# Kernel tuning notes

Hardware: AMD Instinct MI355X
Metric: run time of the kernel (lower is better)

## Reference

```python
import jax, jax.numpy as jnp
import numpy as np

NUM_HEADS = 8
KERNEL = 7  # odd, dilation = 1


def _neighbor_indices(n, k):
    # NATTEN semantics: window start clamped so the kxk window stays inside [0, n)
    r = k // 2
    starts = jnp.clip(jnp.arange(n) - r, 0, n - k)  # [n]
    return starts[:, None] + jnp.arange(k)[None, :]  # [n, k]


def setup_inputs() -> dict:
    key = jax.random.key(0)
    k1, k2, k3, k4 = jax.random.split(key, 4)
    B, H, W, C = 2, 56, 56, 256
    return {
        "x": jax.random.normal(k1, (B, H, W, C), dtype=jnp.float32),
        "w_qk": jax.random.normal(k2, (2 * C, C), dtype=jnp.float32) * 0.02,
        "w_v": jax.random.normal(k3, (C, C), dtype=jnp.float32) * 0.02,
        "w_proj": jax.random.normal(k4, (C, C), dtype=jnp.float32) * 0.02,
        "b_proj": jnp.zeros((C,), dtype=jnp.float32),
    }


def reference(x, w_qk, w_v, w_proj, b_proj):
    B, H, W, C = x.shape
    NH, K = NUM_HEADS, KERNEL
    HD = C // NH
    scale = HD ** -0.5

    # qk / v projections (torch Linear: y = x @ W.T)
    qk = (x @ w_qk.T).reshape(B, H, W, 2, NH, HD)
    q = jnp.moveaxis(qk[:, :, :, 0], 3, 1) * scale  # [B, NH, H, W, HD]
    k = jnp.moveaxis(qk[:, :, :, 1], 3, 1)          # [B, NH, H, W, HD]
    v = jnp.moveaxis((x @ w_v.T).reshape(B, H, W, NH, HD), 3, 1)  # [B, NH, H, W, HD]

    idx_h = _neighbor_indices(H, K)  # [H, K]
    idx_w = _neighbor_indices(W, K)  # [W, K]
    ih = idx_h[:, None, :, None]  # [H, 1, K, 1]
    iw = idx_w[None, :, None, :]  # [1, W, 1, K]

    # Gather per-pixel neighborhoods: [B, NH, H, W, K, K, HD]
    k_nb = k[:, :, ih, iw, :]
    v_nb = v[:, :, ih, iw, :]

    # windowed QK^T -> [B, NH, H, W, K*K]
    attn = jnp.einsum('bnijf,bnijpqf->bnijpq', q, k_nb).reshape(B, NH, H, W, K * K)
    attn = jax.nn.softmax(attn, axis=-1)

    # windowed AV -> [B, NH, H, W, HD]
    out = jnp.einsum('bnijk,bnijkf->bnijf', attn, v_nb.reshape(B, NH, H, W, K * K, HD))

    out = jnp.moveaxis(out, 1, 3).reshape(B, H, W, C)
    out = out @ w_proj.T + b_proj
    return out, attn
```

## Files before the change

### kernel.cpp

```cpp
#include <hip/hip_runtime.h>
#include <math.h>

#define Bb   2
#define Hh   56
#define Ww   56
#define Cc   256
#define NHh  8
#define HDd  32
#define KK   7
#define HWsz (Hh*Ww)
#define Mtot (Bb*Hh*Ww)

typedef __bf16 bf16x8 __attribute__((ext_vector_type(8)));
typedef float  f32x4  __attribute__((ext_vector_type(4)));

__global__ __launch_bounds__(256) void gemm_bf16(
    const float* __restrict__ A, const float* __restrict__ W0,
    const float* __restrict__ W1, float* __restrict__ Cout,
    int Kdim, int N, int n_split, int scale_below, float scale,
    const float* __restrict__ bias)
{
    __shared__ __bf16 As[4096];
    __shared__ __bf16 Bs[4096];

    const int tid = threadIdx.x;
    const int m0  = blockIdx.y * 64;
    const int n0  = blockIdx.x * 64;

    const int mm = tid >> 2;
    const int q  = tid & 3;
    const float* arow = A + (size_t)(m0 + mm) * Kdim + q * 16;
    const int n_idx = n0 + mm;
    const float* brow = (n_idx < n_split ? W0 + (size_t)n_idx * Kdim
                                         : W1 + (size_t)(n_idx - n_split) * Kdim) + q * 16;

    const int ks_st  = q >> 1;
    const int sub_st = mm >> 4;
    const int row_st = mm & 15;
    const int c0_st  = (q & 1) * 2;
    const int blk_st = ks_st * 4 + sub_st;
    const int off0 = blk_st * 512 + row_st * 32 + ((c0_st ^ (row_st & 3)) * 8);
    const int off1 = blk_st * 512 + row_st * 32 + (((c0_st + 1) ^ (row_st & 3)) * 8);

    const int w    = tid >> 6;
    const int lane = tid & 63;
    const int fr_row = lane & 15;
    const int fr_c   = lane >> 4;
    const int fr_off = fr_row * 32 + ((fr_c ^ (fr_row & 3)) * 8);

    f32x4 acc[4] = {};

    for (int k0 = 0; k0 < Kdim; k0 += 64) {
        float4 a0 = *(const float4*)(arow + k0);
        float4 a1 = *(const float4*)(arow + k0 + 4);
        float4 a2 = *(const float4*)(arow + k0 + 8);
        float4 a3 = *(const float4*)(arow + k0 + 12);
        float4 b0 = *(const float4*)(brow + k0);
        float4 b1 = *(const float4*)(brow + k0 + 4);
        float4 b2 = *(const float4*)(brow + k0 + 8);
        float4 b3 = *(const float4*)(brow + k0 + 12);
        __syncthreads();
        bf16x8 av0 = { (__bf16)a0.x, (__bf16)a0.y, (__bf16)a0.z, (__bf16)a0.w,
                       (__bf16)a1.x, (__bf16)a1.y, (__bf16)a1.z, (__bf16)a1.w };
        bf16x8 av1 = { (__bf16)a2.x, (__bf16)a2.y, (__bf16)a2.z, (__bf16)a2.w,
                       (__bf16)a3.x, (__bf16)a3.y, (__bf16)a3.z, (__bf16)a3.w };
        bf16x8 bv0 = { (__bf16)b0.x, (__bf16)b0.y, (__bf16)b0.z, (__bf16)b0.w,
                       (__bf16)b1.x, (__bf16)b1.y, (__bf16)b1.z, (__bf16)b1.w };
        bf16x8 bv1 = { (__bf16)b2.x, (__bf16)b2.y, (__bf16)b2.z, (__bf16)b2.w,
                       (__bf16)b3.x, (__bf16)b3.y, (__bf16)b3.z, (__bf16)b3.w };
        *(bf16x8*)&As[off0] = av0;
        *(bf16x8*)&As[off1] = av1;
        *(bf16x8*)&Bs[off0] = bv0;
        *(bf16x8*)&Bs[off1] = bv1;
        __syncthreads();
        #pragma unroll
        for (int ks = 0; ks < 2; ++ks) {
            bf16x8 af = *(const bf16x8*)&As[(ks * 4 + w) * 512 + fr_off];
            #pragma unroll
            for (int n = 0; n < 4; ++n) {
                bf16x8 bfr = *(const bf16x8*)&Bs[(ks * 4 + n) * 512 + fr_off];
                acc[n] = __builtin_amdgcn_mfma_f32_16x16x32_bf16(af, bfr, acc[n], 0, 0, 0);
            }
        }
    }

    #pragma unroll
    for (int n = 0; n < 4; ++n) {
        const int gcol = n0 + n * 16 + fr_row;
        const float sc_ = (gcol < scale_below) ? scale : 1.f;
        const float bs_ = bias ? bias[gcol] : 0.f;
        #pragma unroll
        for (int r = 0; r < 4; ++r) {
            const int grow = m0 + w * 16 + fr_c * 4 + r;
            Cout[(size_t)grow * N + gcol] = acc[n][r] * sc_ + bs_;
        }
    }
}

__global__ __launch_bounds__(256, 5) void nattn_84(
    const float* __restrict__ qkv, float* __restrict__ attn_out,
    float* __restrict__ attn_glob)
{
    __shared__ float Ks[140 * 36];
    __shared__ float Ss[32 * 49];

    const int bx   = blockIdx.x;
    const int head = bx & 7;
    int t = bx >> 3;
    const int tj = t % 14; t /= 14;
    const int ti = t % 7;
    const int b  = t / 7;
    const int tid = threadIdx.x;

    int base_h = ti * 8 - 3; if (base_h < 0) base_h = 0; if (base_h > Hh - 14) base_h = Hh - 14;
    int base_w = tj * 4 - 3; if (base_w < 0) base_w = 0; if (base_w > Ww - 10) base_w = Ww - 10;

    const int pixb = b * HWsz;
    const int hoff = head * 32;

    #pragma unroll
    for (int it = 0; it < 5; ++it) {
        const int idx = tid + it * 256;
        if (idx < 1120) {
            const int p = idx >> 3, c = idx & 7;
            const int pix = pixb + (base_h + p / 10) * Ww + base_w + p % 10;
            *(float4*)&Ks[p * 36 + c * 4] =
                *(const float4*)&qkv[(size_t)pix * 768 + 256 + hoff + c * 4];
        }
    }

    const int q  = tid >> 3;
    const int r  = tid & 7;
    const int qi = ti * 8 + (q >> 2);
    const int qj = tj * 4 + (q & 3);

    float4 qreg[8];
    {
        const float* qp = &qkv[(size_t)(pixb + qi * Ww + qj) * 768 + hoff];
        #pragma unroll
        for (int c = 0; c < 8; ++c) qreg[c] = *(const float4*)(qp + c * 4);
    }

    float4 vreg[5];
    #pragma unroll
    for (int it = 0; it < 5; ++it) {
        const int idx = tid + it * 256;
        if (idx < 1120) {
            const int p = idx >> 3, c = idx & 7;
            const int pix = pixb + (base_h + p / 10) * Ww + base_w + p % 10;
            vreg[it] = *(const float4*)&qkv[(size_t)pix * 768 + 512 + hoff + c * 4];
        }
    }
    __syncthreads();

    int ih0 = qi - 3; if (ih0 < 0) ih0 = 0; if (ih0 > Hh - 7) ih0 = Hh - 7;
    int iw0 = qj - 3; if (iw0 < 0) iw0 = 0; if (iw0 > Ww - 7) iw0 = Ww - 7;
    const int lh0 = ih0 - base_h, lw0 = iw0 - base_w;

    float sc[7];
    float mx = -1e30f;
    #pragma unroll
    for (int tt = 0; tt < 7; ++tt) {
        const int k = r + 8 * tt;
        if (k < 49) {
            const int krow = (lh0 + k / 7) * 10 + lw0 + k % 7;
            const float* kp = &Ks[krow * 36];
            float acc = 0.f;
            #pragma unroll
            for (int c = 0; c < 8; ++c) {
                const float4 kv = *(const float4*)(kp + c * 4);
                acc += qreg[c].x * kv.x + qreg[c].y * kv.y
                     + qreg[c].z * kv.z + qreg[c].w * kv.w;
            }
            sc[tt] = acc;
            mx = fmaxf(mx, acc);
        }
    }
    mx = fmaxf(mx, __shfl_xor(mx, 1));
    mx = fmaxf(mx, __shfl_xor(mx, 2));
    mx = fmaxf(mx, __shfl_xor(mx, 4));
    float sum = 0.f;
    #pragma unroll
    for (int tt = 0; tt < 7; ++tt) {
        const int k = r + 8 * tt;
        if (k < 49) { sc[tt] = __expf(sc[tt] - mx); sum += sc[tt]; }
    }
    sum += __shfl_xor(sum, 1);
    sum += __shfl_xor(sum, 2);
    sum += __shfl_xor(sum, 4);
    const float inv = 1.f / sum;
    #pragma unroll
    for (int tt = 0; tt < 7; ++tt) {
        const int k = r + 8 * tt;
        if (k < 49) Ss[q * 49 + k] = sc[tt] * inv;
    }
    __syncthreads();

    #pragma unroll
    for (int it = 0; it < 5; ++it) {
        const int idx = tid + it * 256;
        if (idx < 1120) {
            const int p = idx >> 3, c = idx & 7;
            *(float4*)&Ks[p * 36 + c * 4] = vreg[it];
        }
    }
    const size_t agbase = (size_t)(b * NHh + head) * HWsz;
    for (int idx = tid; idx < 32 * 49; idx += 256) {
        const int qq = idx / 49, k = idx - qq * 49;
        attn_glob[(agbase + (ti * 8 + (qq >> 2)) * Ww + tj * 4 + (qq & 3)) * 49 + k]
            = Ss[qq * 49 + k];
    }
    __syncthreads();

    const int d0 = r * 4;
    float4 a0 = {0, 0, 0, 0};
    #pragma unroll
    for (int k = 0; k < 49; ++k) {
        const float pr = Ss[q * 49 + k];
        const int vrow = (lh0 + k / 7) * 10 + lw0 + k % 7;
        const float4 v0 = *(const float4*)&Ks[vrow * 36 + d0];
        a0.x += pr * v0.x; a0.y += pr * v0.y; a0.z += pr * v0.z; a0.w += pr * v0.w;
    }
    float* op = attn_out + (size_t)(pixb + qi * Ww + qj) * 256 + hoff + d0;
    *(float4*)op = a0;
}

extern "C" void kernel_launch(void* const* d_in, const int* in_sizes, int n_in,
                              void* d_out, int out_size, void* d_ws, size_t ws_size,
                              hipStream_t stream)
{
    const float* x      = (const float*)d_in[0];
    const float* w_qk   = (const float*)d_in[1];
    const float* w_v    = (const float*)d_in[2];
    const float* w_proj = (const float*)d_in[3];
    const float* b_proj = (const float*)d_in[4];

    float* out       = (float*)d_out;
    float* attn_glob = out + (size_t)Mtot * Cc;

    float* qkv_ws  = (float*)d_ws;
    float* attn_ws = qkv_ws + (size_t)Mtot * 768;

    const float scale = 0.17677669529663687f;

    gemm_bf16<<<dim3(768 / 64, Mtot / 64), 256, 0, stream>>>(
        x, w_qk, w_v, qkv_ws, Cc, 768, 512, 256, scale, nullptr);

    nattn_84<<<Bb * 7 * 14 * NHh, 256, 0, stream>>>(qkv_ws, attn_ws, attn_glob);

    gemm_bf16<<<dim3(256 / 64, Mtot / 64), 256, 0, stream>>>(
        attn_ws, w_proj, w_proj, out, Cc, Cc, 1 << 30, 0, 1.f, b_proj);
}
```

Before: 117.9 us.

## Store K/V tiles in LDS as bf16 and split AV loop across lane pairs

The neighborhood-attention kernel now keeps its K and V tiles in shared memory as bf16 instead of fp32, halving LDS footprint and the per-thread load/store counts. The AV accumulation is restructured so each lane handles 8 channels over half the 49 neighbors, and the two halves are combined with a shuffle. This cuts LDS traffic and may raise occupancy, at the cost of bf16 rounding of K and V values in the attention scores and output.

```diff
diff --git a/kernel.cpp b/kernel.cpp
--- a/kernel.cpp
+++ b/kernel.cpp
@@ -12,6 +12,7 @@
 #define Mtot (Bb*Hh*Ww)
 
 typedef __bf16 bf16x8 __attribute__((ext_vector_type(8)));
+typedef __bf16 bf16x4 __attribute__((ext_vector_type(4)));
 typedef float  f32x4  __attribute__((ext_vector_type(4)));
 
 __global__ __launch_bounds__(256) void gemm_bf16(
@@ -101,7 +102,7 @@
     const float* __restrict__ qkv, float* __restrict__ attn_out,
     float* __restrict__ attn_glob)
 {
-    __shared__ float Ks[140 * 36];
+    __shared__ __align__(16) __bf16 Ks[140 * 40];
     __shared__ float Ss[32 * 49];
 
     const int bx   = blockIdx.x;
@@ -119,13 +120,17 @@
     const int hoff = head * 32;
 
     #pragma unroll
-    for (int it = 0; it < 5; ++it) {
+    for (int it = 0; it < 3; ++it) {
         const int idx = tid + it * 256;
-        if (idx < 1120) {
-            const int p = idx >> 3, c = idx & 7;
+        if (idx < 560) {
+            const int p = idx >> 2, c = idx & 3;
             const int pix = pixb + (base_h + p / 10) * Ww + base_w + p % 10;
-            *(float4*)&Ks[p * 36 + c * 4] =
-                *(const float4*)&qkv[(size_t)pix * 768 + 256 + hoff + c * 4];
+            const float* kp = &qkv[(size_t)pix * 768 + 256 + hoff + c * 8];
+            float4 k0 = *(const float4*)kp;
+            float4 k1 = *(const float4*)(kp + 4);
+            bf16x8 kb = { (__bf16)k0.x, (__bf16)k0.y, (__bf16)k0.z, (__bf16)k0.w,
+                          (__bf16)k1.x, (__bf16)k1.y, (__bf16)k1.z, (__bf16)k1.w };
+            *(bf16x8*)&Ks[p * 40 + c * 8] = kb;
         }
     }
 
@@ -134,21 +139,27 @@
     const int qi = ti * 8 + (q >> 2);
     const int qj = tj * 4 + (q & 3);
 
-    float4 qreg[8];
+    float qreg[32];
     {
         const float* qp = &qkv[(size_t)(pixb + qi * Ww + qj) * 768 + hoff];
         #pragma unroll
-        for (int c = 0; c < 8; ++c) qreg[c] = *(const float4*)(qp + c * 4);
-    }
-
-    float4 vreg[5];
-    #pragma unroll
-    for (int it = 0; it < 5; ++it) {
+        for (int c = 0; c < 8; ++c) {
+            float4 qv = *(const float4*)(qp + c * 4);
+            qreg[c * 4 + 0] = qv.x; qreg[c * 4 + 1] = qv.y;
+            qreg[c * 4 + 2] = qv.z; qreg[c * 4 + 3] = qv.w;
+        }
+    }
+
+    float4 vreg[6];
+    #pragma unroll
+    for (int it = 0; it < 3; ++it) {
         const int idx = tid + it * 256;
-        if (idx < 1120) {
-            const int p = idx >> 3, c = idx & 7;
+        if (idx < 560) {
+            const int p = idx >> 2, c = idx & 3;
             const int pix = pixb + (base_h + p / 10) * Ww + base_w + p % 10;
-            vreg[it] = *(const float4*)&qkv[(size_t)pix * 768 + 512 + hoff + c * 4];
+            const float* vp = &qkv[(size_t)pix * 768 + 512 + hoff + c * 8];
+            vreg[it * 2]     = *(const float4*)vp;
+            vreg[it * 2 + 1] = *(const float4*)(vp + 4);
         }
     }
     __syncthreads();
@@ -164,13 +175,14 @@
         const int k = r + 8 * tt;
         if (k < 49) {
             const int krow = (lh0 + k / 7) * 10 + lw0 + k % 7;
-            const float* kp = &Ks[krow * 36];
+            const __bf16* kp = &Ks[krow * 40];
             float acc = 0.f;
             #pragma unroll
-            for (int c = 0; c < 8; ++c) {
-                const float4 kv = *(const float4*)(kp + c * 4);
-                acc += qreg[c].x * kv.x + qreg[c].y * kv.y
-                     + qreg[c].z * kv.z + qreg[c].w * kv.w;
+            for (int c = 0; c < 4; ++c) {
+                bf16x8 kv = *(const bf16x8*)(kp + c * 8);
+                #pragma unroll
+                for (int j = 0; j < 8; ++j)
+                    acc += qreg[c * 8 + j] * (float)kv[j];
             }
             sc[tt] = acc;
             mx = fmaxf(mx, acc);
@@ -197,11 +209,14 @@
     __syncthreads();
 
     #pragma unroll
-    for (int it = 0; it < 5; ++it) {
+    for (int it = 0; it < 3; ++it) {
         const int idx = tid + it * 256;
-        if (idx < 1120) {
-            const int p = idx >> 3, c = idx & 7;
-            *(float4*)&Ks[p * 36 + c * 4] = vreg[it];
+        if (idx < 560) {
+            const int p = idx >> 2, c = idx & 3;
+            const float4 v0 = vreg[it * 2], v1 = vreg[it * 2 + 1];
+            bf16x8 vb = { (__bf16)v0.x, (__bf16)v0.y, (__bf16)v0.z, (__bf16)v0.w,
+                          (__bf16)v1.x, (__bf16)v1.y, (__bf16)v1.z, (__bf16)v1.w };
+            *(bf16x8*)&Ks[p * 40 + c * 8] = vb;
         }
     }
     const size_t agbase = (size_t)(b * NHh + head) * HWsz;
@@ -212,17 +227,28 @@
     }
     __syncthreads();
 
-    const int d0 = r * 4;
-    float4 a0 = {0, 0, 0, 0};
-    #pragma unroll
-    for (int k = 0; k < 49; ++k) {
-        const float pr = Ss[q * 49 + k];
-        const int vrow = (lh0 + k / 7) * 10 + lw0 + k % 7;
-        const float4 v0 = *(const float4*)&Ks[vrow * 36 + d0];
-        a0.x += pr * v0.x; a0.y += pr * v0.y; a0.z += pr * v0.z; a0.w += pr * v0.w;
-    }
-    float* op = attn_out + (size_t)(pixb + qi * Ww + qj) * 256 + hoff + d0;
-    *(float4*)op = a0;
+    const int rc  = r & 3;
+    const int par = r >> 2;
+    float a[8] = {};
+    #pragma unroll
+    for (int tt = 0; tt < 25; ++tt) {
+        const int k = par + 2 * tt;
+        if (k < 49) {
+            const float pr = Ss[q * 49 + k];
+            const int vrow = (lh0 + k / 7) * 10 + lw0 + k % 7;
+            bf16x8 v8 = *(const bf16x8*)&Ks[vrow * 40 + rc * 8];
+            #pragma unroll
+            for (int j = 0; j < 8; ++j)
+                a[j] += pr * (float)v8[j];
+        }
+    }
+    #pragma unroll
+    for (int j = 0; j < 8; ++j) a[j] += __shfl_xor(a[j], 4);
+
+    float4 o;
+    o.x = a[par * 4 + 0]; o.y = a[par * 4 + 1];
+    o.z = a[par * 4 + 2]; o.w = a[par * 4 + 3];
+    *(float4*)(attn_out + (size_t)(pixb + qi * Ww + qj) * 256 + hoff + rc * 8 + par * 4) = o;
 }
 
 extern "C" void kernel_launch(void* const* d_in, const int* in_sizes, int n_in,
```

New measurement: 113.2 us. -4.0%, faster.
